# Performance work log

Hardware: AMD Instinct MI355X
Metric: run time of the kernel (lower is better)

The kernel has to match this reference:

```python
import jax, jax.numpy as jnp
import numpy as np

B, I, H = 16384, 1024, 1024

def setup_inputs() -> dict:
    key = jax.random.key(0)
    ks = jax.random.split(key, 7)
    scale = 0.02  # small init so gates are not saturated
    return {
        "x": jax.random.normal(ks[0], (B, I), jnp.float32),
        "h_prev": jax.random.normal(ks[1], (B, H), jnp.float32),
        "c_prev": jax.random.normal(ks[2], (B, H), jnp.float32),
        "Wx": jax.random.normal(ks[3], (4, H, I), jnp.float32) * scale,  # order: z,i,f,o
        "bx": jnp.zeros((4, H), jnp.float32),
        "Rh": jax.random.normal(ks[4], (4, H, H), jnp.float32) * scale,
        "bh": jnp.zeros((4, H), jnp.float32),
    }

def reference(x, h_prev, c_prev, Wx, bx, Rh, bh):
    # Fused form of 4 input-GEMMs + 4 recurrent-GEMMs: two einsums over stacked gates.
    # gate order g=0..3 -> z, i, f, o
    pre = (jnp.einsum('bi,ghi->bgh', x, Wx) + bx[None]
           + jnp.einsum('bh,gkh->bgk', h_prev, Rh) + bh[None])  # [B,4,H]
    z = jnp.tanh(pre[:, 0])
    i = jax.nn.sigmoid(pre[:, 1])
    f = jax.nn.sigmoid(pre[:, 2])
    o = jax.nn.sigmoid(pre[:, 3])
    c = f * c_prev + i * z
    h = o * jnp.tanh(c)
    return (h, c)
```

## Files before the change

### kernel.cpp

```cpp
#include <hip/hip_runtime.h>
#include <hip/hip_bf16.h>
#include <stdint.h>


typedef __attribute__((ext_vector_type(8))) short bf16x8;
typedef __attribute__((ext_vector_type(4))) float f32x4;
typedef __attribute__((ext_vector_type(8))) unsigned short u16x8;

#define AS1 __attribute__((address_space(1)))
#define AS3 __attribute__((address_space(3)))

constexpr int BATCH = 16384;
constexpr int HDIM  = 1024;
constexpr int KDIM  = 2048;
constexpr int NDIM  = 4096;

__device__ inline unsigned short f2bf(float f) {
  uint32_t u = __builtin_bit_cast(uint32_t, f);
  u += 0x7fffu + ((u >> 16) & 1u);
  return (unsigned short)(u >> 16);
}
__device__ inline u16x8 cvt8(const float* __restrict__ src) {
  float4 f0 = *(const float4*)src;
  float4 f1 = *(const float4*)(src + 4);
  u16x8 v;
  v[0] = f2bf(f0.x); v[1] = f2bf(f0.y); v[2] = f2bf(f0.z); v[3] = f2bf(f0.w);
  v[4] = f2bf(f1.x); v[5] = f2bf(f1.y); v[6] = f2bf(f1.z); v[7] = f2bf(f1.w);
  return v;
}
__device__ inline float sigmoid_f(float x) {
  float e = __builtin_amdgcn_exp2f(-1.4426950408889634f * x);
  return __builtin_amdgcn_rcpf(1.0f + e);
}
__device__ inline float tanh_f(float x) {
  float e = __builtin_amdgcn_exp2f(2.8853900817779268f * x);
  return 1.0f - 2.0f * __builtin_amdgcn_rcpf(1.0f + e);
}

__global__ void pack_xh(const float* __restrict__ x, const float* __restrict__ hp,
                        unsigned short* __restrict__ xh) {
  const int64_t nch = (int64_t)BATCH * KDIM / 8;
  for (int64_t c = (int64_t)blockIdx.x * blockDim.x + threadIdx.x; c < nch;
       c += (int64_t)gridDim.x * blockDim.x) {
    const int b = (int)(c >> 8);
    const int k = ((int)c & 255) * 8;
    const float* src = (k < 1024) ? (x + (int64_t)b * 1024 + k)
                                  : (hp + (int64_t)b * 1024 + (k - 1024));
    *(u16x8*)(xh + c * 8) = cvt8(src);
  }
}
__global__ void pack_w(const float* __restrict__ Wx, const float* __restrict__ Rh,
                       unsigned short* __restrict__ wp) {
  const int64_t nch = (int64_t)NDIM * KDIM / 8;
  for (int64_t c = (int64_t)blockIdx.x * blockDim.x + threadIdx.x; c < nch;
       c += (int64_t)gridDim.x * blockDim.x) {
    const int np = (int)(c >> 8);
    const int k = ((int)c & 255) * 8;
    const int h = np >> 2, g = np & 3;
    const float* src = (k < 1024) ? (Wx + (int64_t)(g * HDIM + h) * 1024 + k)
                                  : (Rh + (int64_t)(g * HDIM + h) * 1024 + (k - 1024));
    *(u16x8*)(wp + c * 8) = cvt8(src);
  }
}
__global__ void pack_bias(const float* __restrict__ bx, const float* __restrict__ bh,
                          float* __restrict__ bias) {
  int n = blockIdx.x * blockDim.x + threadIdx.x;
  if (n < NDIM) {
    int h = n >> 2, g = n & 3;
    bias[n] = bx[g * HDIM + h] + bh[g * HDIM + h];
  }
}

template <int OFF>
__device__ __forceinline__ bf16x8 dsb128(uint32_t a) {
  bf16x8 r;
  asm volatile("ds_read_b128 %0, %1 offset:%2" : "=v"(r) : "v"(a), "i"(OFF) : "memory");
  return r;
}

#define BARR   asm volatile("s_barrier" ::: "memory")
#define LGKM0  asm volatile("s_waitcnt lgkmcnt(0)" ::: "memory")
#define VM6    asm volatile("s_waitcnt vmcnt(6)" ::: "memory")
#define VM0    asm volatile("s_waitcnt vmcnt(0)" ::: "memory")
#define SCHED0 __builtin_amdgcn_sched_barrier(0)

#define READ_A(BUF, KH, MH) { constexpr int _o = (BUF)*32768 + (KH)*16384 + (MH)*4096; \
  fa[0] = dsb128<_o>(av); fa[1] = dsb128<_o+1024>(av);                                  \
  fa[2] = dsb128<_o+2048>(av); fa[3] = dsb128<_o+3072>(av); }
#define READ_B(BUF, KH) { constexpr int _o = (BUF)*32768 + (KH)*16384; \
  fb[0] = dsb128<_o>(bv); fb[1] = dsb128<_o+1024>(bv);                  \
  fb[2] = dsb128<_o+2048>(bv); fb[3] = dsb128<_o+3072>(bv); }

#define MFMA16(MB) { \
  __builtin_amdgcn_s_setprio(1); \
  _Pragma("unroll") for (int j = 0; j < 4; ++j) \
  _Pragma("unroll") for (int ni = 0; ni < 4; ++ni) \
    acc[(MB)*4 + j][ni] = __builtin_amdgcn_mfma_f32_16x16x32_bf16(fa[j], fb[ni], acc[(MB)*4 + j][ni], 0, 0, 0); \
  __builtin_amdgcn_s_setprio(0); }

#define STAGE(SRC, DOFF) { \
  __builtin_amdgcn_global_load_lds((const AS1 void*)(SRC), (AS3 void*)(dstL + (DOFF)), 16, 0, 0); \
  __builtin_amdgcn_global_load_lds((const AS1 void*)((SRC) + 524288), (AS3 void*)(dstL + (DOFF) + 8192), 16, 0, 0); }

__global__ __launch_bounds__(512, 2) void lstm_gemm(
    const unsigned short* __restrict__ XH, const unsigned short* __restrict__ Wp,
    const float* __restrict__ bias, const float* __restrict__ c_prev,
    float* __restrict__ out_h, float* __restrict__ out_c) {
  __shared__ __align__(1024) char smem_[131072];

  const int tid  = threadIdx.x;
  const int l    = tid & 63;
  const int w    = tid >> 6;
  const int wr   = w >> 2, wc = w & 3;
  const int la   = l & 15;
  const int kg   = l >> 4;

  const int xcd = blockIdx.x & 7;
  const int q   = blockIdx.x >> 3;
  const int tn  = xcd * 2 + (q & 1);
  const int tm  = q >> 1;
  const int m0  = tm * 256;
  const int n0  = tn * 256;

  const int rbase = w * 16 + (l >> 2);
  const int ck    = (l & 3) ^ ((l >> 3) & 3);
  const char* pA = (const char*)XH + (int64_t)(m0 + rbase) * 4096 + ck * 16;
  const char* pB = (const char*)Wp + (int64_t)(n0 + rbase) * 4096 + ck * 16;
  char* dstL = smem_ + w * 1024;

  const int cc = kg ^ ((la >> 1) & 3);
  const uint32_t lds0 = (uint32_t)(uintptr_t)(AS3 char*)smem_;
  const uint32_t av = lds0 + wr * 8192 + la * 64 + cc * 16;
  const uint32_t bv = lds0 + 65536 + wc * 4096 + la * 64 + cc * 16;

  f32x4 acc[8][4] = {};
  bf16x8 fa[4], fb[4];

  STAGE(pB,       65536);
  STAGE(pA,       0);
  STAGE(pB + 64,  81920);
  STAGE(pA + 64,  16384);
  STAGE(pB + 128, 98304);
  STAGE(pA + 128, 32768);
  STAGE(pB + 192, 114688);
  VM6; BARR;

#pragma unroll 1
  for (int it = 0; it < 16; ++it) {
    int kt2 = 2 * it + 2; if (kt2 > 31) kt2 = 31;
    int kt3 = 2 * it + 3; if (kt3 > 31) kt3 = 31;
    const char* sA1 = pA + (2 * it + 1) * 128;
    const char* sA2 = pA + kt2 * 128;
    const char* sA3 = pA + kt3 * 128;
    const char* sB2 = pB + kt2 * 128;
    const char* sB3 = pB + kt3 * 128;

    READ_B(0, 0) READ_A(0, 0, 0)
    STAGE(sA1 + 64, 49152);
    BARR; LGKM0; SCHED0; MFMA16(0) BARR;
    READ_A(0, 0, 1)
    STAGE(sB2, 65536);
    BARR; LGKM0; SCHED0; MFMA16(1) BARR;
    READ_B(0, 1) READ_A(0, 1, 0)
    STAGE(sA2, 0);
    BARR; LGKM0; SCHED0; MFMA16(0) BARR;
    READ_A(0, 1, 1)
    STAGE(sB2 + 64, 81920);
    BARR; LGKM0; SCHED0; MFMA16(1) VM6; BARR;
    READ_B(1, 0) READ_A(1, 0, 0)
    STAGE(sA2 + 64, 16384);
    BARR; LGKM0; SCHED0; MFMA16(0) BARR;
    READ_A(1, 0, 1)
    STAGE(sB3, 98304);
    BARR; LGKM0; SCHED0; MFMA16(1) BARR;
    READ_B(1, 1) READ_A(1, 1, 0)
    STAGE(sA3, 32768);
    BARR; LGKM0; SCHED0; MFMA16(0) BARR;
    READ_A(1, 1, 1)
    STAGE(sB3 + 64, 114688);
    BARR; LGKM0; SCHED0; MFMA16(1) VM6; BARR;
  }

  VM0;
  __syncthreads();
  float* ew = (float*)smem_ + w * 1088;
  const float4 bias4 = *(const float4*)(bias + n0 + wc * 64 + 4 * la);
  const int hg = ((n0 + wc * 64) >> 2) + la;

#pragma unroll
  for (int mi = 0; mi < 8; ++mi) {
#pragma unroll
    for (int ni = 0; ni < 4; ++ni)
#pragma unroll
      for (int r = 0; r < 4; ++r)
        ew[(4 * kg + r) * 68 + ni * 16 + la] = acc[mi][ni][r];
#pragma unroll
    for (int p = 0; p < 4; ++p) {
      const int row = p * 4 + kg;
      float4 g4 = *(const float4*)(ew + row * 68 + 4 * la);
      const int b = m0 + wr * 128 + mi * 16 + row;
      const uint32_t oidx = (uint32_t)b * HDIM + (uint32_t)hg;
      const float cp = c_prev[oidx];
      const float zg = tanh_f(g4.x + bias4.x);
      const float ig = sigmoid_f(g4.y + bias4.y);
      const float fg = sigmoid_f(g4.z + bias4.z);
      const float og = sigmoid_f(g4.w + bias4.w);
      const float cn = fg * cp + ig * zg;
      out_h[oidx] = og * tanh_f(cn);
      out_c[oidx] = cn;
    }
  }
}

extern "C" void kernel_launch(void* const* d_in, const int* in_sizes, int n_in,
                              void* d_out, int out_size, void* d_ws, size_t ws_size,
                              hipStream_t stream) {
  const float* x  = (const float*)d_in[0];
  const float* hp = (const float*)d_in[1];
  const float* cp = (const float*)d_in[2];
  const float* Wx = (const float*)d_in[3];
  const float* bx = (const float*)d_in[4];
  const float* Rh = (const float*)d_in[5];
  const float* bh = (const float*)d_in[6];

  unsigned short* XH = (unsigned short*)d_ws;
  unsigned short* Wp = XH + (size_t)BATCH * KDIM;
  float* bias = (float*)(Wp + (size_t)NDIM * KDIM);
  float* out_h = (float*)d_out;
  float* out_c = out_h + (size_t)BATCH * HDIM;

  pack_xh<<<2048, 256, 0, stream>>>(x, hp, XH);
  pack_w<<<1024, 256, 0, stream>>>(Wx, Rh, Wp);
  pack_bias<<<16, 256, 0, stream>>>(bx, bh, bias);
  lstm_gemm<<<1024, 512, 0, stream>>>(XH, Wp, bias, cp, out_h, out_c);
}
```

Measured before the change: 314.8 us.

## Double-buffer LDS fragment registers to overlap ds_reads with MFMA

Splits the A/B fragment registers into two sets so the LDS reads for the next MFMA block are issued before the current block's MFMAs run. Partial lgkmcnt waits replace full drains, and the barrier count per sub-step drops. The aim is to hide LDS read latency behind matrix math. The cost is more VGPRs under a 512-thread, 2-block launch bound, and the barrier/VM wait placement must still protect the LDS buffers that are being overwritten.

Measured after the change: 306.5 us. -2.6%, faster.

```diff
diff --git a/kernel.cpp b/kernel.cpp
--- a/kernel.cpp
+++ b/kernel.cpp
@@ -79,23 +79,24 @@
 }
 
 #define BARR   asm volatile("s_barrier" ::: "memory")
-#define LGKM0  asm volatile("s_waitcnt lgkmcnt(0)" ::: "memory")
+#define LGKM4  asm volatile("s_waitcnt lgkmcnt(4)" ::: "memory")
+#define LGKM8  asm volatile("s_waitcnt lgkmcnt(8)" ::: "memory")
 #define VM6    asm volatile("s_waitcnt vmcnt(6)" ::: "memory")
 #define VM0    asm volatile("s_waitcnt vmcnt(0)" ::: "memory")
 #define SCHED0 __builtin_amdgcn_sched_barrier(0)
 
-#define READ_A(BUF, KH, MH) { constexpr int _o = (BUF)*32768 + (KH)*16384 + (MH)*4096; \
-  fa[0] = dsb128<_o>(av); fa[1] = dsb128<_o+1024>(av);                                  \
-  fa[2] = dsb128<_o+2048>(av); fa[3] = dsb128<_o+3072>(av); }
-#define READ_B(BUF, KH) { constexpr int _o = (BUF)*32768 + (KH)*16384; \
-  fb[0] = dsb128<_o>(bv); fb[1] = dsb128<_o+1024>(bv);                  \
-  fb[2] = dsb128<_o+2048>(bv); fb[3] = dsb128<_o+3072>(bv); }
-
-#define MFMA16(MB) { \
+#define ISS_A(FA, BUF, KH, MH) { constexpr int _o = (BUF)*32768 + (KH)*16384 + (MH)*4096; \
+  FA[0] = dsb128<_o>(av); FA[1] = dsb128<_o+1024>(av);                                     \
+  FA[2] = dsb128<_o+2048>(av); FA[3] = dsb128<_o+3072>(av); }
+#define ISS_B(FB, BUF, KH) { constexpr int _o = (BUF)*32768 + (KH)*16384; \
+  FB[0] = dsb128<_o>(bv); FB[1] = dsb128<_o+1024>(bv);                     \
+  FB[2] = dsb128<_o+2048>(bv); FB[3] = dsb128<_o+3072>(bv); }
+
+#define MFMA16(FA, FB, MB) { \
   __builtin_amdgcn_s_setprio(1); \
   _Pragma("unroll") for (int j = 0; j < 4; ++j) \
   _Pragma("unroll") for (int ni = 0; ni < 4; ++ni) \
-    acc[(MB)*4 + j][ni] = __builtin_amdgcn_mfma_f32_16x16x32_bf16(fa[j], fb[ni], acc[(MB)*4 + j][ni], 0, 0, 0); \
+    acc[(MB)*4 + j][ni] = __builtin_amdgcn_mfma_f32_16x16x32_bf16(FA[j], FB[ni], acc[(MB)*4 + j][ni], 0, 0, 0); \
   __builtin_amdgcn_s_setprio(0); }
 
 #define STAGE(SRC, DOFF) { \
@@ -134,7 +135,7 @@
   const uint32_t bv = lds0 + 65536 + wc * 4096 + la * 64 + cc * 16;
 
   f32x4 acc[8][4] = {};
-  bf16x8 fa[4], fb[4];
+  bf16x8 fa0[4], fa1[4], fb0[4], fb1[4];
 
   STAGE(pB,       65536);
   STAGE(pA,       0);
@@ -144,6 +145,7 @@
   STAGE(pA + 128, 32768);
   STAGE(pB + 192, 114688);
   VM6; BARR;
+  ISS_B(fb0, 0, 0) ISS_A(fa0, 0, 0, 0)
 
 #pragma unroll 1
   for (int it = 0; it < 16; ++it) {
@@ -155,30 +157,42 @@
     const char* sB2 = pB + kt2 * 128;
     const char* sB3 = pB + kt3 * 128;
 
-    READ_B(0, 0) READ_A(0, 0, 0)
+    BARR;
     STAGE(sA1 + 64, 49152);
-    BARR; LGKM0; SCHED0; MFMA16(0) BARR;
-    READ_A(0, 0, 1)
+    ISS_A(fa1, 0, 0, 1)
+    LGKM4; SCHED0; MFMA16(fa0, fb0, 0)
+    BARR;
     STAGE(sB2, 65536);
-    BARR; LGKM0; SCHED0; MFMA16(1) BARR;
-    READ_B(0, 1) READ_A(0, 1, 0)
+    ISS_B(fb1, 0, 1) ISS_A(fa0, 0, 1, 0)
+    LGKM8; SCHED0; MFMA16(fa1, fb0, 1)
+    VM6;
+    BARR;
     STAGE(sA2, 0);
-    BARR; LGKM0; SCHED0; MFMA16(0) BARR;
-    READ_A(0, 1, 1)
+    ISS_A(fa1, 0, 1, 1)
+    LGKM4; SCHED0; MFMA16(fa0, fb1, 0)
+    BARR;
     STAGE(sB2 + 64, 81920);
-    BARR; LGKM0; SCHED0; MFMA16(1) VM6; BARR;
-    READ_B(1, 0) READ_A(1, 0, 0)
+    ISS_B(fb0, 1, 0) ISS_A(fa0, 1, 0, 0)
+    LGKM8; SCHED0; MFMA16(fa1, fb1, 1)
+    VM6;
+    BARR;
     STAGE(sA2 + 64, 16384);
-    BARR; LGKM0; SCHED0; MFMA16(0) BARR;
-    READ_A(1, 0, 1)
+    ISS_A(fa1, 1, 0, 1)
+    LGKM4; SCHED0; MFMA16(fa0, fb0, 0)
+    BARR;
     STAGE(sB3, 98304);
-    BARR; LGKM0; SCHED0; MFMA16(1) BARR;
-    READ_B(1, 1) READ_A(1, 1, 0)
+    ISS_B(fb1, 1, 1) ISS_A(fa0, 1, 1, 0)
+    LGKM8; SCHED0; MFMA16(fa1, fb0, 1)
+    VM6;
+    BARR;
     STAGE(sA3, 32768);
-    BARR; LGKM0; SCHED0; MFMA16(0) BARR;
-    READ_A(1, 1, 1)
+    ISS_A(fa1, 1, 1, 1)
+    LGKM4; SCHED0; MFMA16(fa0, fb1, 0)
+    BARR;
     STAGE(sB3 + 64, 114688);
-    BARR; LGKM0; SCHED0; MFMA16(1) VM6; BARR;
+    ISS_B(fb0, 0, 0) ISS_A(fa0, 0, 0, 0)
+    LGKM8; SCHED0; MFMA16(fa1, fb1, 1)
+    VM6;
   }
 
   VM0;
```

## Double-buffer LDS fragments in registers to overlap ds_reads with MFMA

Applied to the files above, without the earlier changes.

Restructures the GEMM main loop so each phase issues the next k-half's LDS fragment reads (8 A, 4 B) into a second register set, then runs 32 MFMAs on the previously loaded set, waiting only on lgkmcnt(12). This replaces the earlier pattern of read, wait for all LDS reads, compute, with half the barriers per k-step. The global-to-LDS staging order and vmcnt thresholds are reshuffled to match. It doubles the fragment registers, which may strain the 2-blocks-per-CU launch bound, and it relies on subtle barrier and waitcnt ordering for correctness.

After: 316.6 us. No clear change (+0.6%).

```diff
diff --git a/kernel.cpp b/kernel.cpp
--- a/kernel.cpp
+++ b/kernel.cpp
@@ -78,24 +78,27 @@
   return r;
 }
 
-#define BARR   asm volatile("s_barrier" ::: "memory")
-#define LGKM0  asm volatile("s_waitcnt lgkmcnt(0)" ::: "memory")
-#define VM6    asm volatile("s_waitcnt vmcnt(6)" ::: "memory")
-#define VM0    asm volatile("s_waitcnt vmcnt(0)" ::: "memory")
-#define SCHED0 __builtin_amdgcn_sched_barrier(0)
-
-#define READ_A(BUF, KH, MH) { constexpr int _o = (BUF)*32768 + (KH)*16384 + (MH)*4096; \
-  fa[0] = dsb128<_o>(av); fa[1] = dsb128<_o+1024>(av);                                  \
-  fa[2] = dsb128<_o+2048>(av); fa[3] = dsb128<_o+3072>(av); }
-#define READ_B(BUF, KH) { constexpr int _o = (BUF)*32768 + (KH)*16384; \
-  fb[0] = dsb128<_o>(bv); fb[1] = dsb128<_o+1024>(bv);                  \
-  fb[2] = dsb128<_o+2048>(bv); fb[3] = dsb128<_o+3072>(bv); }
-
-#define MFMA16(MB) { \
+#define BARR    asm volatile("s_barrier" ::: "memory")
+#define LGKM12  asm volatile("s_waitcnt lgkmcnt(12)" ::: "memory")
+#define VM8     asm volatile("s_waitcnt vmcnt(8)" ::: "memory")
+#define VM0     asm volatile("s_waitcnt vmcnt(0)" ::: "memory")
+#define SCHED0  __builtin_amdgcn_sched_barrier(0)
+
+#define ISS_A8(FA, BUF, KH) { constexpr int _o = (BUF)*32768 + (KH)*16384;   \
+  FA[0] = dsb128<_o>(av);      FA[1] = dsb128<_o+1024>(av);                   \
+  FA[2] = dsb128<_o+2048>(av); FA[3] = dsb128<_o+3072>(av);                   \
+  FA[4] = dsb128<_o+4096>(av); FA[5] = dsb128<_o+5120>(av);                   \
+  FA[6] = dsb128<_o+6144>(av); FA[7] = dsb128<_o+7168>(av); }
+#define ISS_B4(FB, BUF, KH) { constexpr int _o = (BUF)*32768 + (KH)*16384;   \
+  FB[0] = dsb128<_o>(bv);      FB[1] = dsb128<_o+1024>(bv);                   \
+  FB[2] = dsb128<_o+2048>(bv); FB[3] = dsb128<_o+3072>(bv); }
+
+#define MFMA32(FA, FB) { \
   __builtin_amdgcn_s_setprio(1); \
-  _Pragma("unroll") for (int j = 0; j < 4; ++j) \
+  _Pragma("unroll") for (int mh = 0; mh < 2; ++mh) \
+  _Pragma("unroll") for (int mi = 0; mi < 4; ++mi) \
   _Pragma("unroll") for (int ni = 0; ni < 4; ++ni) \
-    acc[(MB)*4 + j][ni] = __builtin_amdgcn_mfma_f32_16x16x32_bf16(fa[j], fb[ni], acc[(MB)*4 + j][ni], 0, 0, 0); \
+    acc[mh * 4 + mi][ni] = __builtin_amdgcn_mfma_f32_16x16x32_bf16(FA[mh * 4 + mi], FB[ni], acc[mh * 4 + mi][ni], 0, 0, 0); \
   __builtin_amdgcn_s_setprio(0); }
 
 #define STAGE(SRC, DOFF) { \
@@ -134,7 +137,7 @@
   const uint32_t bv = lds0 + 65536 + wc * 4096 + la * 64 + cc * 16;
 
   f32x4 acc[8][4] = {};
-  bf16x8 fa[4], fb[4];
+  bf16x8 fa0[8], fa1[8], fb0[4], fb1[4];
 
   STAGE(pB,       65536);
   STAGE(pA,       0);
@@ -142,43 +145,47 @@
   STAGE(pA + 64,  16384);
   STAGE(pB + 128, 98304);
   STAGE(pA + 128, 32768);
-  STAGE(pB + 192, 114688);
-  VM6; BARR;
+  VM8; BARR;
+  ISS_B4(fb0, 0, 0) ISS_A8(fa0, 0, 0)
 
 #pragma unroll 1
   for (int it = 0; it < 16; ++it) {
     int kt2 = 2 * it + 2; if (kt2 > 31) kt2 = 31;
     int kt3 = 2 * it + 3; if (kt3 > 31) kt3 = 31;
+    const char* sB1 = pB + (2 * it + 1) * 128;
     const char* sA1 = pA + (2 * it + 1) * 128;
     const char* sA2 = pA + kt2 * 128;
     const char* sA3 = pA + kt3 * 128;
     const char* sB2 = pB + kt2 * 128;
     const char* sB3 = pB + kt3 * 128;
 
-    READ_B(0, 0) READ_A(0, 0, 0)
+    BARR;
+    STAGE(sB1 + 64, 114688);
     STAGE(sA1 + 64, 49152);
-    BARR; LGKM0; SCHED0; MFMA16(0) BARR;
-    READ_A(0, 0, 1)
+    VM8;
+    ISS_B4(fb1, 0, 1) ISS_A8(fa1, 0, 1)
+    LGKM12; SCHED0; MFMA32(fa0, fb0)
+
+    BARR;
     STAGE(sB2, 65536);
-    BARR; LGKM0; SCHED0; MFMA16(1) BARR;
-    READ_B(0, 1) READ_A(0, 1, 0)
     STAGE(sA2, 0);
-    BARR; LGKM0; SCHED0; MFMA16(0) BARR;
-    READ_A(0, 1, 1)
+    VM8;
+    ISS_B4(fb0, 1, 0) ISS_A8(fa0, 1, 0)
+    LGKM12; SCHED0; MFMA32(fa1, fb1)
+
+    BARR;
     STAGE(sB2 + 64, 81920);
-    BARR; LGKM0; SCHED0; MFMA16(1) VM6; BARR;
-    READ_B(1, 0) READ_A(1, 0, 0)
     STAGE(sA2 + 64, 16384);
-    BARR; LGKM0; SCHED0; MFMA16(0) BARR;
-    READ_A(1, 0, 1)
+    VM8;
+    ISS_B4(fb1, 1, 1) ISS_A8(fa1, 1, 1)
+    LGKM12; SCHED0; MFMA32(fa0, fb0)
+
+    BARR;
     STAGE(sB3, 98304);
-    BARR; LGKM0; SCHED0; MFMA16(1) BARR;
-    READ_B(1, 1) READ_A(1, 1, 0)
     STAGE(sA3, 32768);
-    BARR; LGKM0; SCHED0; MFMA16(0) BARR;
-    READ_A(1, 1, 1)
-    STAGE(sB3 + 64, 114688);
-    BARR; LGKM0; SCHED0; MFMA16(1) VM6; BARR;
+    VM8;
+    ISS_B4(fb0, 0, 0) ISS_A8(fa0, 0, 0)
+    LGKM12; SCHED0; MFMA32(fa1, fb1)
   }
 
   VM0;
```
